# Performance work log

Measured on AMD Instinct MI355X. Metric: run time of the kernel, lower is better.

## Reference

```python
import jax, jax.numpy as jnp
import numpy as np

B, F, H, W = 1, 6, 20, 26
S = F * H * W            # 3120 tokens
DIM, NH, HD = 1536, 12, 128
C = HD // 2              # 64 rotary channels
T_C = C - 2 * (C // 3)   # 22 temporal channels
H_C = C // 3             # 21
W_C = C // 3             # 21
LOCAL_FRAMES = 4         # local_attn_size (in frames)
SINK_FRAMES = 1          # sink_size (in frames)
EPS = 1e-6
MAX_POS = 1024


def _angle_table(n_ch):
    inv = 1.0 / (10000.0 ** (np.arange(n_ch, dtype=np.float64) / n_ch))
    return np.outer(np.arange(MAX_POS, dtype=np.float64), inv)


def setup_inputs() -> dict:
    key = jax.random.key(0)
    ks = jax.random.split(key, 8)
    sc = 0.02
    ang = np.concatenate([_angle_table(T_C), _angle_table(H_C), _angle_table(W_C)], axis=1)  # [1024, 64]
    return {
        "x": jax.random.normal(ks[0], (B, S, DIM), jnp.float32),
        "seq_lens": jnp.array([S], jnp.int32),
        "grid_sizes": jnp.array([[F, H, W]], jnp.int32),
        "freqs_cos": jnp.asarray(np.cos(ang), jnp.float32),
        "freqs_sin": jnp.asarray(np.sin(ang), jnp.float32),
        "Wq": jax.random.normal(ks[1], (DIM, DIM), jnp.float32) * sc,
        "bq": jnp.zeros((DIM,), jnp.float32),
        "Wk": jax.random.normal(ks[2], (DIM, DIM), jnp.float32) * sc,
        "bk": jnp.zeros((DIM,), jnp.float32),
        "Wv": jax.random.normal(ks[3], (DIM, DIM), jnp.float32) * sc,
        "bv": jnp.zeros((DIM,), jnp.float32),
        "Wo": jax.random.normal(ks[4], (DIM, DIM), jnp.float32) * sc,
        "bo": jnp.zeros((DIM,), jnp.float32),
        "gq": jnp.ones((DIM,), jnp.float32),
        "gk": jnp.ones((DIM,), jnp.float32),
    }


def _rms_norm(x, g):
    # WanRMSNorm: x * rsqrt(mean(x^2) + eps) * weight
    return x * jax.lax.rsqrt(jnp.mean(x * x, axis=-1, keepdims=True) + EPS) * g


def _rope_apply(x, freqs_cos, freqs_sin):
    # x: [B, S, NH, HD]; per-token 3D (f,h,w) rotary on consecutive pairs.
    pos = jnp.arange(S)
    f = pos // (H * W)
    hh = (pos // W) % H
    ww = pos % W
    cos_t, cos_h, cos_w = freqs_cos[:, :T_C], freqs_cos[:, T_C:T_C + H_C], freqs_cos[:, T_C + H_C:]
    sin_t, sin_h, sin_w = freqs_sin[:, :T_C], freqs_sin[:, T_C:T_C + H_C], freqs_sin[:, T_C + H_C:]
    cos = jnp.concatenate([cos_t[f], cos_h[hh], cos_w[ww]], axis=-1)[None, :, None, :]  # [1,S,1,C]
    sin = jnp.concatenate([sin_t[f], sin_h[hh], sin_w[ww]], axis=-1)[None, :, None, :]
    xp = x.reshape(B, S, NH, C, 2)
    xr, xi = xp[..., 0], xp[..., 1]
    out = jnp.stack([xr * cos - xi * sin, xr * sin + xi * cos], axis=-1)
    return out.reshape(B, S, NH, HD)


def _block_mask():
    # frame-causal + local window (in frames) + sink frames: [S, S] bool
    fid = jnp.arange(S) // (H * W)
    fi, fj = fid[:, None], fid[None, :]
    return (fj <= fi) & ((fi - fj < LOCAL_FRAMES) | (fj < SINK_FRAMES))


def reference(x, seq_lens, grid_sizes, freqs_cos, freqs_sin,
              Wq, bq, Wk, bk, Wv, bv, Wo, bo, gq, gk):
    q = _rms_norm(x @ Wq + bq, gq).reshape(B, S, NH, HD)
    k = _rms_norm(x @ Wk + bk, gk).reshape(B, S, NH, HD)
    v = (x @ Wv + bv).reshape(B, S, NH, HD)
    rq = _rope_apply(q, freqs_cos, freqs_sin)
    rk = _rope_apply(k, freqs_cos, freqs_sin)
    scale = 1.0 / jnp.sqrt(jnp.asarray(HD, x.dtype))
    scores = jnp.einsum('bind,bjnd->bnij', rq, rk) * scale  # [B,NH,S,S]
    scores = jnp.where(_block_mask()[None, None], scores, jnp.finfo(scores.dtype).min)
    attn = jax.nn.softmax(scores, axis=-1)
    out = jnp.einsum('bnij,bjnd->bind', attn, v).reshape(B, S, DIM)
    return out @ Wo + bo
```

## Files before the change

### kernel.cpp

```cpp
#include <hip/hip_runtime.h>
#include <hip/hip_bf16.h>
#include <stdint.h>

typedef short v8s __attribute__((ext_vector_type(8)));
typedef short v4h __attribute__((ext_vector_type(4)));
typedef float v4f __attribute__((ext_vector_type(4)));
typedef unsigned short u16;

#define S_LEN 3120
#define DIMN 1536
#define NHEAD 12
#define HDIM 128
#define FRM 520
#define NT64 49
#define T64_PH 166
#define TOT64 1992
#define NSTEP32 17
#define SCALE_QK 0.088388347648318447f
#define MAXOFF 12.0f

struct TaskMap {
  unsigned char tile[T64_PH];
  unsigned char frame[T64_PH];
  short accv[NT64];
  unsigned char nf[NT64];
};
constexpr TaskMap make_map() {
  TaskMap m{};
  int acc = 0;
  for (int tile = 0; tile < NT64; ++tile) {
    int q0t = tile * 64;
    int f_lo = q0t / FRM;
    int qhi = q0t + 63 < S_LEN - 1 ? q0t + 63 : S_LEN - 1;
    int f_hi = qhi / FRM;
    int fstart = f_lo - 3 > 0 ? f_lo - 3 : 0;
    int sink = fstart > 0 ? 1 : 0;
    int nf = f_hi - fstart + 1 + sink;
    m.accv[tile] = (short)acc;
    m.nf[tile] = (unsigned char)nf;
    for (int c = 0; c < nf; ++c) {
      m.tile[acc + c] = (unsigned char)tile;
      m.frame[acc + c] = (unsigned char)(sink ? (c == 0 ? 0 : fstart + c - 1) : (fstart + c));
    }
    acc += nf;
  }
  return m;
}
__device__ __constant__ TaskMap TM = make_map();

__device__ __forceinline__ v4f mfma16(v8s a, v8s b, v4f c) {
  return __builtin_amdgcn_mfma_f32_16x16x32_bf16(a, b, c, 0, 0, 0);
}
__device__ __forceinline__ float b2f(u16 u) {
  union { float f; unsigned int i; } x; x.i = ((unsigned int)u) << 16; return x.f;
}
__device__ __forceinline__ u16 f2b(float f) {
  union { float f; unsigned int i; } x; x.f = f;
  unsigned int r = x.i + 0x7FFFu + ((x.i >> 16) & 1u);
  return (u16)(r >> 16);
}
__device__ __forceinline__ void async16(const void* g, void* l) {
  __builtin_amdgcn_global_load_lds(
      (__attribute__((address_space(1))) const void*)g,
      (__attribute__((address_space(3))) void*)l, 16, 0, 0);
}

__global__ void detect_dtype(const u16* __restrict__ w, int* __restrict__ flag) {
  __shared__ int sh;
  int t = threadIdx.x;
  if (t == 0) sh = 0;
  __syncthreads();
  u16 m0 = (u16)(w[2 * t] & 0x7FFF);
  u16 m1 = (u16)(w[2 * t + 1] & 0x7FFF);
  if (m0 >= 0x4480 || m1 >= 0x4480) atomicOr(&sh, 1);
  __syncthreads();
  if (t == 0) *flag = sh;
}

struct PrepArgs {
  const void* tin[4]; u16* tout[4];
  const void* csrc[9]; u16* cdst[9]; int cn[9];
};
__global__ __launch_bounds__(256) void prep(PrepArgs a, const int* __restrict__ flag) {
  int isf = *flag;
  int z = blockIdx.z;
  int t = threadIdx.x;
  int bidx = blockIdx.y * gridDim.x + blockIdx.x;
  if (z < 4) {
    __shared__ u16 tile[32][33];
    const float* inf = (const float*)a.tin[z];
    const u16* inb = (const u16*)a.tin[z];
    u16* out = a.tout[z];
    int tx = t & 31, ty = t >> 5;
    int gr0 = blockIdx.y * 32, gc0 = blockIdx.x * 32;
#pragma unroll
    for (int i = 0; i < 4; ++i) {
      int r = ty + i * 8;
      size_t idx = (size_t)(gr0 + r) * DIMN + gc0 + tx;
      tile[r][tx] = isf ? f2b(inf[idx]) : inb[idx];
    }
    __syncthreads();
#pragma unroll
    for (int i = 0; i < 4; ++i) {
      int r = ty + i * 8;
      out[(size_t)(gc0 + r) * DIMN + gr0 + tx] = tile[tx][r];
    }
  } else {
    int id = z - 4;
    int n4 = a.cn[id] >> 2;
    const float* sf = (const float*)a.csrc[id];
    const u16* sb = (const u16*)a.csrc[id];
    u16* d = a.cdst[id];
    int stride = gridDim.x * gridDim.y * 256;
    for (int i = bidx * 256 + t; i < n4; i += stride) {
      v4h o;
      if (isf) {
        float4 x4 = *(const float4*)(sf + (size_t)i * 4);
        o[0] = (short)f2b(x4.x); o[1] = (short)f2b(x4.y);
        o[2] = (short)f2b(x4.z); o[3] = (short)f2b(x4.w);
      } else {
        o = *(const v4h*)(sb + (size_t)i * 4);
      }
      *(v4h*)(d + (size_t)i * 4) = o;
    }
  }
}

template <int MT, int NT>
__global__ __launch_bounds__(256) void gemm3(
    const u16* __restrict__ A,
    const u16* BT0, const u16* BT1, const u16* BT2,
    const u16* b0, const u16* b1, const u16* b2,
    void* C0, void* C1, void* C2, int M, const int* __restrict__ flag, int dyn) {
  static_assert(MT == 64, "4-wave layout assumes MT==64");
  const u16* BT; const u16* bias; void* C;
  if (blockIdx.z == 0)      { BT = BT0; bias = b0; C = C0; }
  else if (blockIdx.z == 1) { BT = BT1; bias = b1; C = C1; }
  else                      { BT = BT2; bias = b2; C = C2; }
  int f32out = dyn ? *flag : 0;
  __shared__ __align__(16) short As[MT * 64];
  __shared__ __align__(16) short Bs[NT * 64];
  int t = threadIdx.x, w = t >> 6, l = t & 63;
  int ln = l & 15, lg = l >> 4;
  int m0 = blockIdx.y * MT, n0 = blockIdx.x * NT;
  int lr = l >> 3;
  int gl = (l & 7) ^ lr;
  constexpr int ACH = MT / 32;
  constexpr int BCH = NT / 32;
  const u16* gAp[ACH]; short* lAp[ACH];
#pragma unroll
  for (int i = 0; i < ACH; ++i) {
    int c = w * ACH + i;
    int arow = min(m0 + c * 8 + lr, M - 1);
    gAp[i] = A + (size_t)arow * DIMN + gl * 8;
    lAp[i] = As + c * 512;
  }
  const u16* gBp[BCH]; short* lBp[BCH];
#pragma unroll
  for (int i = 0; i < BCH; ++i) {
    int c = w * BCH + i;
    int brow = n0 + c * 8 + lr;
    gBp[i] = BT + (size_t)brow * DIMN + gl * 8;
    lBp[i] = Bs + c * 512;
  }
  constexpr int NJ = NT / 64;
  int aoff[2][4], boff[2][NJ];
#pragma unroll
  for (int ks = 0; ks < 2; ++ks) {
#pragma unroll
    for (int i = 0; i < 4; ++i) {
      int ar = i * 16 + ln;
      aoff[ks][i] = ar * 64 + (((ks * 4 + lg) ^ (ar & 7)) * 8);
    }
#pragma unroll
    for (int j = 0; j < NJ; ++j) {
      int br = w * (NJ * 16) + j * 16 + ln;
      boff[ks][j] = br * 64 + (((ks * 4 + lg) ^ (br & 7)) * 8);
    }
  }
  v4f acc[4][NJ] = {};
  for (int k0 = 0; k0 < DIMN; k0 += 64) {
    __syncthreads();
#pragma unroll
    for (int i = 0; i < ACH; ++i) async16(gAp[i] + k0, lAp[i]);
#pragma unroll
    for (int i = 0; i < BCH; ++i) async16(gBp[i] + k0, lBp[i]);
    __syncthreads();
#pragma unroll
    for (int ks = 0; ks < 2; ++ks) {
      v8s af[4], bfr[NJ];
#pragma unroll
      for (int i = 0; i < 4; ++i) af[i] = *(const v8s*)(As + aoff[ks][i]);
#pragma unroll
      for (int j = 0; j < NJ; ++j) bfr[j] = *(const v8s*)(Bs + boff[ks][j]);
#pragma unroll
      for (int i = 0; i < 4; ++i)
#pragma unroll
        for (int j = 0; j < NJ; ++j) acc[i][j] = mfma16(af[i], bfr[j], acc[i][j]);
    }
  }
  if ((!dyn) && blockIdx.z == 2) {
#pragma unroll
    for (int i = 0; i < 4; ++i) {
      int rb = m0 + i * 16 + lg * 4;
      if (rb + 3 >= M) continue;
#pragma unroll
      for (int j = 0; j < NJ; ++j) {
        int col = n0 + w * (NJ * 16) + j * 16 + ln;
        float bv = b2f(bias[col]);
        v4h pk;
#pragma unroll
        for (int r = 0; r < 4; ++r) pk[r] = (short)f2b(acc[i][j][r] + bv);
        *(v4h*)((u16*)C + (size_t)col * S_LEN + rb) = pk;
      }
    }
    return;
  }
#pragma unroll
  for (int i = 0; i < 4; ++i) {
    int rb = m0 + i * 16 + lg * 4;
#pragma unroll
    for (int j = 0; j < NJ; ++j) {
      int col = n0 + w * (NJ * 16) + j * 16 + ln;
      float bv = b2f(bias[col]);
#pragma unroll
      for (int r = 0; r < 4; ++r) {
        int grow = rb + r;
        if (grow < M) {
          size_t idx = (size_t)grow * DIMN + col;
          float val = acc[i][j][r] + bv;
          if (f32out) ((float*)C)[idx] = val;
          else        ((u16*)C)[idx] = f2b(val);
        }
      }
    }
  }
}

__global__ __launch_bounds__(256) void norm_rope(u16* __restrict__ Q, u16* __restrict__ K,
                                                 const u16* __restrict__ gq,
                                                 const u16* __restrict__ gk,
                                                 const u16* __restrict__ fcos,
                                                 const u16* __restrict__ fsin) {
  int t = threadIdx.x, w = t >> 6, l = t & 63;
  int s = blockIdx.x * 4 + w;
  u16* base = (blockIdx.y == 0 ? Q : K) + (size_t)s * DIMN;
  const u16* g = (blockIdx.y == 0) ? gq : gk;
  v8s xv[3], gv[3];
#pragma unroll
  for (int c = 0; c < 3; ++c) {
    xv[c] = *(const v8s*)(base + c * 512 + l * 8);
    gv[c] = *(const v8s*)(g + c * 512 + l * 8);
  }
  float x[24];
  float ss = 0.f;
#pragma unroll
  for (int c = 0; c < 3; ++c)
#pragma unroll
    for (int j = 0; j < 8; ++j) {
      float v = b2f((u16)xv[c][j]);
      x[c * 8 + j] = v;
      ss += v * v;
    }
#pragma unroll
  for (int off = 32; off > 0; off >>= 1) ss += __shfl_xor(ss, off);
  float rs = rsqrtf(ss * (1.0f / DIMN) + 1e-6f);
  int f = s / FRM;
  int hh = (s / 26) % 20;
  int ww = s % 26;
#pragma unroll
  for (int c = 0; c < 3; ++c) {
    v8s out;
#pragma unroll
    for (int u = 0; u < 4; ++u) {
      int e0 = c * 512 + l * 8 + 2 * u;
      int ch = (e0 & 127) >> 1;
      int p = (ch < 22) ? f : ((ch < 43) ? hh : ww);
      float co = b2f(fcos[p * 64 + ch]);
      float si = b2f(fsin[p * 64 + ch]);
      float xr = x[c * 8 + 2 * u] * rs * b2f((u16)gv[c][2 * u]);
      float xi = x[c * 8 + 2 * u + 1] * rs * b2f((u16)gv[c][2 * u + 1]);
      out[2 * u]     = (short)f2b(xr * co - xi * si);
      out[2 * u + 1] = (short)f2b(xr * si + xi * co);
    }
    *(v8s*)(base + c * 512 + l * 8) = out;
  }
}

__global__ __launch_bounds__(256) void attn_block(const u16* __restrict__ Q,
                                                  const u16* __restrict__ K,
                                                  const u16* __restrict__ VT,
                                                  u16* __restrict__ Po,
                                                  float* __restrict__ Pl) {
  __shared__ __align__(16) short Ks[2][32 * 128];
  __shared__ __align__(16) short Vs[2][128 * 32];
  __shared__ __align__(16) short Pt[4][16 * 40];
  int t = threadIdx.x, w = t >> 6, l = t & 63;
  int ln = l & 15, lg = l >> 4;
  int task = blockIdx.x;
  int head = task / T64_PH, tid = task % T64_PH;
  int tile = TM.tile[tid], frame = TM.frame[tid];
  int q0 = tile * 64 + w * 16;
  v8s qf[4];
  bool rowok[4];
  {
    int row = min(q0 + ln, S_LEN - 1);
    const u16* qp = Q + (size_t)row * DIMN + head * HDIM + lg * 8;
#pragma unroll
    for (int c = 0; c < 4; ++c) qf[c] = *(const v8s*)(qp + c * 32);
#pragma unroll
    for (int r = 0; r < 4; ++r) {
      int qr = q0 + lg * 4 + r;
      int fi = (qr < S_LEN) ? qr / FRM : -1;
      rowok[r] = (frame <= fi) && ((fi - frame) < 4 || frame == 0);
    }
  }
  float lsum[4] = {};
  v4f o[8] = {};
  int kbeg = frame * FRM, kend = kbeg + FRM;
  int kr_i[2], kgl_i[2], vd_i[2], vgl_i[2];
#pragma unroll
  for (int i = 0; i < 2; ++i) {
    int n = (w * 2 + i) * 64 + l;
    kr_i[i] = n >> 4;
    kgl_i[i] = (n & 15) ^ (kr_i[i] & 15);
    vd_i[i] = n >> 2;
    vgl_i[i] = (n & 3) ^ (vd_i[i] & 3);
  }
  const u16* Kb = K + head * HDIM;
  {
    int kb = kbeg;
#pragma unroll
    for (int i = 0; i < 2; ++i) {
      int krow = min(kb + kr_i[i], S_LEN - 1);
      async16(Kb + (size_t)krow * DIMN + kgl_i[i] * 8,
              (char*)Ks + (size_t)(w * 2 + i) * 1024);
      async16(VT + (size_t)(head * HDIM + vd_i[i]) * S_LEN + kb + vgl_i[i] * 8,
              (char*)Vs + (size_t)(w * 2 + i) * 1024);
    }
  }
  __syncthreads();
  for (int it = 0; it < NSTEP32; ++it) {
    int cur = it & 1;
    if (it + 1 < NSTEP32) {
      int kbn = kbeg + (it + 1) * 32;
      size_t boff = (size_t)(cur ^ 1) * 8192;
#pragma unroll
      for (int i = 0; i < 2; ++i) {
        int krow = min(kbn + kr_i[i], S_LEN - 1);
        async16(Kb + (size_t)krow * DIMN + kgl_i[i] * 8,
                (char*)Ks + boff + (size_t)(w * 2 + i) * 1024);
        async16(VT + (size_t)(head * HDIM + vd_i[i]) * S_LEN + kbn + vgl_i[i] * 8,
                (char*)Vs + boff + (size_t)(w * 2 + i) * 1024);
      }
    }
    int kb = kbeg + it * 32;
    v4f s[2] = {};
    __builtin_amdgcn_s_setprio(1);
#pragma unroll
    for (int kg = 0; kg < 2; ++kg) {
#pragma unroll
      for (int c = 0; c < 4; ++c) {
        v8s kf = *(const v8s*)(&Ks[cur][(kg * 16 + ln) * 128 + (((c * 4 + lg) ^ ln) * 8)]);
        s[kg] = mfma16(qf[c], kf, s[kg]);
      }
    }
    __builtin_amdgcn_s_setprio(0);
#pragma unroll
    for (int kg = 0; kg < 2; ++kg) {
      bool jv = (kb + kg * 16 + ln) < kend;
#pragma unroll
      for (int r = 0; r < 4; ++r) {
        float p = (rowok[r] && jv) ? __expf(s[kg][r] * SCALE_QK - MAXOFF) : 0.f;
        unsigned int bi = __float_as_uint(p) & 0xffff0000u;
        lsum[r] += __uint_as_float(bi);
        Pt[w][(lg * 4 + r) * 40 + kg * 16 + ln] = (u16)(bi >> 16);
      }
    }
    v8s pf0 = *(const v8s*)(&Pt[w][ln * 40 + lg * 8]);
    __builtin_amdgcn_s_setprio(1);
#pragma unroll
    for (int d = 0; d < 8; ++d) {
      int rr = d * 16 + ln;
      v8s vf = *(const v8s*)(&Vs[cur][rr * 32 + ((lg ^ (rr & 3)) * 8)]);
      o[d] = mfma16(pf0, vf, o[d]);
    }
    __builtin_amdgcn_s_setprio(0);
    __syncthreads();
  }
#pragma unroll
  for (int r = 0; r < 4; ++r) {
    float v = lsum[r];
    v += __shfl_xor(v, 1);
    v += __shfl_xor(v, 2);
    v += __shfl_xor(v, 4);
    v += __shfl_xor(v, 8);
    lsum[r] = v;
  }
  size_t pbase = (size_t)task * (64 * 128);
#pragma unroll
  for (int d = 0; d < 8; ++d)
#pragma unroll
    for (int r = 0; r < 4; ++r) {
      int lrow = w * 16 + lg * 4 + r;
      Po[pbase + lrow * 128 + d * 16 + ln] = f2b(o[d][r]);
    }
  if (ln == 0) {
#pragma unroll
    for (int r = 0; r < 4; ++r)
      Pl[task * 64 + w * 16 + lg * 4 + r] = lsum[r];
  }
}

__global__ __launch_bounds__(256) void attn_combine(const u16* __restrict__ Po,
                                                    const float* __restrict__ Pl,
                                                    u16* __restrict__ Oa) {
  int tile = blockIdx.x, h = blockIdx.y;
  int accv = TM.accv[tile], nf = TM.nf[tile];
  int base = h * T64_PH + accv;
  int t = threadIdx.x;
  int row = t >> 2, seg = (t & 3) * 32;
  int grow = tile * 64 + row;
  if (grow >= S_LEN) return;
  float lsum = 0.f;
  float ao[32];
#pragma unroll
  for (int j = 0; j < 32; ++j) ao[j] = 0.f;
  for (int c = 0; c < nf; ++c) {
    int task = base + c;
    lsum += Pl[task * 64 + row];
    const u16* p = Po + (size_t)task * 8192 + row * 128 + seg;
#pragma unroll
    for (int v = 0; v < 4; ++v) {
      v8s x = *(const v8s*)(p + v * 8);
#pragma unroll
      for (int j = 0; j < 8; ++j) ao[v * 8 + j] += b2f((u16)x[j]);
    }
  }
  float inv = 1.0f / lsum;
  u16* dst = Oa + (size_t)grow * DIMN + h * HDIM + seg;
#pragma unroll
  for (int v = 0; v < 4; ++v) {
    v8s res;
#pragma unroll
    for (int j = 0; j < 8; ++j) res[j] = (short)f2b(ao[v * 8 + j] * inv);
    *(v8s*)(dst + v * 8) = res;
  }
}

extern "C" void kernel_launch(void* const* d_in, const int* in_sizes, int n_in,
                              void* d_out, int out_size, void* d_ws, size_t ws_size,
                              hipStream_t stream) {
  (void)n_in; (void)out_size; (void)ws_size;
  int* flag = (int*)d_ws;
  u16* ws = (u16*)d_ws;
  size_t off = 16;
  const size_t SD = (size_t)S_LEN * DIMN;
  const size_t WW = (size_t)DIMN * DIMN;
  const size_t NPO = (size_t)1032 * 128 * 128;
  auto alloc = [&](size_t n) { u16* p = ws + off; off += (n + 7) & ~(size_t)7; return p; };
  u16* Xc  = alloc(SD);
  u16* Fc  = alloc(65536);
  u16* Fs  = alloc(65536);
  u16* bqc = alloc(1536); u16* bkc = alloc(1536); u16* bvc = alloc(1536); u16* boc = alloc(1536);
  u16* gqc = alloc(1536); u16* gkc = alloc(1536);
  u16* Qr = alloc(SD); u16* Kr = alloc(SD);
  u16* VT = alloc(SD);
  u16* Oa = alloc(SD);
  u16* WoT = alloc(WW);
  u16* WqT = alloc(WW); u16* WkT = alloc(WW); u16* WvT = alloc(WW);
  alloc(NPO - 3 * WW);
  float* Pl = (float*)alloc((size_t)TOT64 * 64 * 2);
  u16* Po = WqT;

  detect_dtype<<<1, 256, 0, stream>>>((const u16*)d_in[5], flag);

  PrepArgs pa;
  pa.tin[0] = d_in[5];  pa.tout[0] = WqT;
  pa.tin[1] = d_in[7];  pa.tout[1] = WkT;
  pa.tin[2] = d_in[9];  pa.tout[2] = WvT;
  pa.tin[3] = d_in[11]; pa.tout[3] = WoT;
  const int srcIdx[9] = {0, 3, 4, 6, 8, 10, 12, 13, 14};
  u16* dsts[9] = {Xc, Fc, Fs, bqc, bkc, bvc, boc, gqc, gkc};
  for (int i = 0; i < 9; ++i) {
    pa.csrc[i] = d_in[srcIdx[i]];
    pa.cdst[i] = dsts[i];
    pa.cn[i] = in_sizes[srcIdx[i]];
  }
  dim3 b256(256);
  prep<<<dim3(48, 48, 13), b256, 0, stream>>>(pa, flag);
  gemm3<64, 128><<<dim3(12, 49, 3), b256, 0, stream>>>(Xc, WqT, WkT, WvT, bqc, bkc, bvc,
                                                       Qr, Kr, VT, S_LEN, flag, 0);
  norm_rope<<<dim3(S_LEN / 4, 2), b256, 0, stream>>>(Qr, Kr, gqc, gkc, Fc, Fs);
  attn_block<<<dim3(TOT64), dim3(256), 0, stream>>>(Qr, Kr, VT, Po, Pl);
  attn_combine<<<dim3(NT64, NHEAD), b256, 0, stream>>>(Po, Pl, Oa);
  gemm3<64, 128><<<dim3(12, 49, 1), b256, 0, stream>>>(Oa, WoT, WoT, WoT, boc, boc, boc,
                                                       d_out, d_out, d_out, S_LEN, flag, 1);
}
```

Measured before the change: 344.1 us.

## Double-buffer LDS tiles in gemm3 to overlap global loads with MFMA

The projection GEMM now keeps two LDS buffers for the A and B tiles and issues the async loads for the next K-step before computing on the current one. It waits with a hand-written vmcnt count and raw s_barrier instead of two __syncthreads per iteration. The goal is to hide global-to-LDS latency behind the MFMA work. In exchange it doubles LDS use, which may lower occupancy. The hardcoded vmcnt(6) is only correct when each stage issues exactly six loads, so it depends on the tile sizes used.

```diff
diff --git a/kernel.cpp b/kernel.cpp
--- a/kernel.cpp
+++ b/kernel.cpp
@@ -138,8 +138,10 @@
   else if (blockIdx.z == 1) { BT = BT1; bias = b1; C = C1; }
   else                      { BT = BT2; bias = b2; C = C2; }
   int f32out = dyn ? *flag : 0;
-  __shared__ __align__(16) short As[MT * 64];
-  __shared__ __align__(16) short Bs[NT * 64];
+  constexpr int ABUF = MT * 64;
+  constexpr int BBUF = NT * 64;
+  __shared__ __align__(16) short As[2 * ABUF];
+  __shared__ __align__(16) short Bs[2 * BBUF];
   int t = threadIdx.x, w = t >> 6, l = t & 63;
   int ln = l & 15, lg = l >> 4;
   int m0 = blockIdx.y * MT, n0 = blockIdx.x * NT;
@@ -179,25 +181,39 @@
     }
   }
   v4f acc[4][NJ] = {};
-  for (int k0 = 0; k0 < DIMN; k0 += 64) {
-    __syncthreads();
-#pragma unroll
-    for (int i = 0; i < ACH; ++i) async16(gAp[i] + k0, lAp[i]);
-#pragma unroll
-    for (int i = 0; i < BCH; ++i) async16(gBp[i] + k0, lBp[i]);
-    __syncthreads();
+  constexpr int NK = DIMN / 64;
+#pragma unroll
+  for (int i = 0; i < ACH; ++i) async16(gAp[i], lAp[i]);
+#pragma unroll
+  for (int i = 0; i < BCH; ++i) async16(gBp[i], lBp[i]);
+  for (int it = 0; it < NK; ++it) {
+    int cur = it & 1;
+    int ab = cur * ABUF, bb = cur * BBUF;
+    if (it + 1 < NK) {
+      int k0n = (it + 1) * 64;
+      int nb = cur ^ 1;
+#pragma unroll
+      for (int i = 0; i < ACH; ++i) async16(gAp[i] + k0n, lAp[i] + nb * ABUF);
+#pragma unroll
+      for (int i = 0; i < BCH; ++i) async16(gBp[i] + k0n, lBp[i] + nb * BBUF);
+      asm volatile("s_waitcnt vmcnt(6)" ::: "memory");
+    } else {
+      asm volatile("s_waitcnt vmcnt(0)" ::: "memory");
+    }
+    asm volatile("s_barrier" ::: "memory");
 #pragma unroll
     for (int ks = 0; ks < 2; ++ks) {
       v8s af[4], bfr[NJ];
 #pragma unroll
-      for (int i = 0; i < 4; ++i) af[i] = *(const v8s*)(As + aoff[ks][i]);
-#pragma unroll
-      for (int j = 0; j < NJ; ++j) bfr[j] = *(const v8s*)(Bs + boff[ks][j]);
+      for (int i = 0; i < 4; ++i) af[i] = *(const v8s*)(As + ab + aoff[ks][i]);
+#pragma unroll
+      for (int j = 0; j < NJ; ++j) bfr[j] = *(const v8s*)(Bs + bb + boff[ks][j]);
 #pragma unroll
       for (int i = 0; i < 4; ++i)
 #pragma unroll
         for (int j = 0; j < NJ; ++j) acc[i][j] = mfma16(af[i], bfr[j], acc[i][j]);
     }
+    asm volatile("s_barrier" ::: "memory");
   }
   if ((!dyn) && blockIdx.z == 2) {
 #pragma unroll
```

Result: slower. 352.2 us (+2.3%).
